# Kernel tuning notes

Measured on AMD Instinct MI355X. Metric: run time of the kernel, lower is better.

The kernel has to match this reference:

```python
import jax, jax.numpy as jnp
import numpy as np


def setup_inputs() -> dict:
    key = jax.random.key(0)
    k1, k2 = jax.random.split(key)
    decoder_state_t = jax.random.normal(k1, (32, 256), dtype=jnp.float32)
    encoder_states = jax.random.normal(k2, (32, 8192, 256), dtype=jnp.float32)
    return {"decoder_state_t": decoder_state_t, "encoder_states": encoder_states}


def reference(decoder_state_t, encoder_states):
    # score[b, s] = sum_h decoder_state_t[b, h] * encoder_states[b, s, h]
    score = jnp.einsum("bh,bsh->bs", decoder_state_t, encoder_states)
    atten_prob = jax.nn.softmax(score, axis=-1)            # (bs, source_length)
    # context[b, h] = sum_s atten_prob[b, s] * encoder_states[b, s, h]
    context = jnp.einsum("bs,bsh->bh", atten_prob, encoder_states)
    return (atten_prob, context)
```

## Files before the change

kernel.cpp:

```cpp
#include <hip/hip_runtime.h>
#include <math.h>

#define B_ 32
#define S_ 8192
#define H_ 256
#define CHUNK_ 512
#define WAVES_PB 4
#define WROWS (CHUNK_ / WAVES_PB)
#define TILE_ 16
#define NCHUNK (S_ / CHUNK_)
#define NPART (B_ * NCHUNK * WAVES_PB)
#define PPB (NCHUNK * WAVES_PB)

__global__ __launch_bounds__(256) void
k1_flash(const float* __restrict__ dec, const float* __restrict__ enc,
         float* __restrict__ scores_out, float* __restrict__ pm,
         float* __restrict__ pl, float* __restrict__ pc) {
    const int lane  = threadIdx.x & 63;
    const int wave  = threadIdx.x >> 6;
    const int batch = blockIdx.x >> 4;
    const int chunk = blockIdx.x & (NCHUNK - 1);
    const int rowBase = chunk * CHUNK_ + wave * WROWS;

    const float4 d = *(const float4*)(dec + batch * H_ + lane * 4);
    const float* ebase = enc + (size_t)batch * S_ * H_;

    float  m = -INFINITY, l = 0.f;
    float4 c = make_float4(0.f, 0.f, 0.f, 0.f);

    for (int t = 0; t < WROWS / TILE_; ++t) {
        const int r0 = rowBase + t * TILE_;
        float4 v[TILE_];
        float  sc[TILE_];
#pragma unroll
        for (int r = 0; r < TILE_; ++r) {
            v[r] = *(const float4*)(ebase + (size_t)(r0 + r) * H_ + lane * 4);
            float sp = v[r].x * d.x + v[r].y * d.y + v[r].z * d.z + v[r].w * d.w;
#pragma unroll
            for (int off = 32; off; off >>= 1) sp += __shfl_xor(sp, off);
            sc[r] = sp;
        }
        float tmax = sc[0];
#pragma unroll
        for (int r = 1; r < TILE_; ++r) tmax = fmaxf(tmax, sc[r]);
        const float mnew = fmaxf(m, tmax);
        const float f = __expf(m - mnew);
        c.x *= f; c.y *= f; c.z *= f; c.w *= f;
        l *= f;
        m = mnew;
#pragma unroll
        for (int r = 0; r < TILE_; ++r) {
            const float p = __expf(sc[r] - m);
            l += p;
            c.x += p * v[r].x;
            c.y += p * v[r].y;
            c.z += p * v[r].z;
            c.w += p * v[r].w;
        }
        if (lane == 0) {
            float* so = scores_out + batch * S_ + r0;
            *(float4*)(so + 0)  = make_float4(sc[0],  sc[1],  sc[2],  sc[3]);
            *(float4*)(so + 4)  = make_float4(sc[4],  sc[5],  sc[6],  sc[7]);
            *(float4*)(so + 8)  = make_float4(sc[8],  sc[9],  sc[10], sc[11]);
            *(float4*)(so + 12) = make_float4(sc[12], sc[13], sc[14], sc[15]);
        }
    }

    const int pid = blockIdx.x * WAVES_PB + wave;
    *(float4*)(pc + (size_t)pid * H_ + lane * 4) = c;
    if (lane == 0) { pm[pid] = m; pl[pid] = l; }
}

__global__ __launch_bounds__(256) void
k23_finish(const float* __restrict__ pm, const float* __restrict__ pl,
           const float* __restrict__ pc, float* __restrict__ probs,
           float* __restrict__ ctx_out) {
    const int lane = threadIdx.x & 63;

    if (blockIdx.x < 256) {
        const int b = blockIdx.x >> 3;
        const float pmv = pm[b * PPB + lane];
        const float plv = pl[b * PPB + lane];
        float M = pmv;
#pragma unroll
        for (int off = 32; off; off >>= 1) M = fmaxf(M, __shfl_xor(M, off));
        float Lp = __expf(pmv - M) * plv;
#pragma unroll
        for (int off = 32; off; off >>= 1) Lp += __shfl_xor(Lp, off);
        const float R = 1.f / Lp;

        float* p = probs + b * S_ + (blockIdx.x & 7) * 1024 + threadIdx.x * 4;
        float4 v = *(const float4*)p;
        v.x = __expf(v.x - M) * R;
        v.y = __expf(v.y - M) * R;
        v.z = __expf(v.z - M) * R;
        v.w = __expf(v.w - M) * R;
        *(float4*)p = v;
    } else {
        const int b = blockIdx.x - 256;
        const int h = threadIdx.x;
        const float pmv = pm[b * PPB + lane];
        const float plv = pl[b * PPB + lane];
        float M = pmv;
#pragma unroll
        for (int off = 32; off; off >>= 1) M = fmaxf(M, __shfl_xor(M, off));
        const float w = __expf(pmv - M);
        float L = w * plv;
#pragma unroll
        for (int off = 32; off; off >>= 1) L += __shfl_xor(L, off);

        float acc = 0.f;
        const float* pcb = pc + (size_t)b * PPB * H_ + h;
#pragma unroll 8
        for (int i = 0; i < PPB; ++i) {
            acc += __shfl(w, i) * pcb[(size_t)i * H_];
        }
        ctx_out[b * H_ + h] = acc / L;
    }
}

extern "C" void kernel_launch(void* const* d_in, const int* in_sizes, int n_in,
                              void* d_out, int out_size, void* d_ws, size_t ws_size,
                              hipStream_t stream) {
    const float* dec = (const float*)d_in[0];
    const float* enc = (const float*)d_in[1];
    float* out    = (float*)d_out;
    float* scores = out;
    float* ctx    = out + B_ * S_;

    float* pm = (float*)d_ws;
    float* pl = pm + NPART;
    float* pc = pl + NPART;

    k1_flash<<<B_ * NCHUNK, 256, 0, stream>>>(dec, enc, scores, pm, pl, pc);
    k23_finish<<<256 + B_, 256, 0, stream>>>(pm, pl, pc, scores, ctx);
}
```

Measured before the change: 52.15 us.

## Fuse flash partial pass and finish into one cooperative kernel with grid sync

Merges the two kernels into a single cooperative launch. A grid-wide barrier separates the partial softmax/context pass from the normalization and context reduction, and each block then normalizes its own chunk of probabilities while chunk-0 blocks reduce the context through shared memory. This removes the second launch and the inter-kernel gap. In exchange it adds the cost of the grid barrier and the cooperative launch, and the 512-block grid must be co-resident for the barrier to work.

```diff
diff --git a/kernel.cpp b/kernel.cpp
--- a/kernel.cpp
+++ b/kernel.cpp
@@ -1,5 +1,8 @@
 #include <hip/hip_runtime.h>
+#include <hip/hip_cooperative_groups.h>
 #include <math.h>
+
+namespace cg = cooperative_groups;
 
 #define B_ 32
 #define S_ 8192
@@ -12,10 +15,11 @@
 #define NPART (B_ * NCHUNK * WAVES_PB)
 #define PPB (NCHUNK * WAVES_PB)
 
-__global__ __launch_bounds__(256) void
-k1_flash(const float* __restrict__ dec, const float* __restrict__ enc,
-         float* __restrict__ scores_out, float* __restrict__ pm,
-         float* __restrict__ pl, float* __restrict__ pc) {
+__global__ __launch_bounds__(256, 2) void
+k_coop(const float* __restrict__ dec, const float* __restrict__ enc,
+       float* __restrict__ probs, float* __restrict__ ctx_out,
+       float* __restrict__ pm, float* __restrict__ pl,
+       float* __restrict__ pc) {
     const int lane  = threadIdx.x & 63;
     const int wave  = threadIdx.x >> 6;
     const int batch = blockIdx.x >> 4;
@@ -58,7 +62,7 @@
             c.w += p * v[r].w;
         }
         if (lane == 0) {
-            float* so = scores_out + batch * S_ + r0;
+            float* so = probs + batch * S_ + r0;
             *(float4*)(so + 0)  = make_float4(sc[0],  sc[1],  sc[2],  sc[3]);
             *(float4*)(so + 4)  = make_float4(sc[4],  sc[5],  sc[6],  sc[7]);
             *(float4*)(so + 8)  = make_float4(sc[8],  sc[9],  sc[10], sc[11]);
@@ -69,53 +73,54 @@
     const int pid = blockIdx.x * WAVES_PB + wave;
     *(float4*)(pc + (size_t)pid * H_ + lane * 4) = c;
     if (lane == 0) { pm[pid] = m; pl[pid] = l; }
-}
 
-__global__ __launch_bounds__(256) void
-k23_finish(const float* __restrict__ pm, const float* __restrict__ pl,
-           const float* __restrict__ pc, float* __restrict__ probs,
-           float* __restrict__ ctx_out) {
-    const int lane = threadIdx.x & 63;
+    cg::this_grid().sync();
 
-    if (blockIdx.x < 256) {
-        const int b = blockIdx.x >> 3;
-        const float pmv = pm[b * PPB + lane];
-        const float plv = pl[b * PPB + lane];
-        float M = pmv;
+    const float pmv = pm[batch * PPB + lane];
+    const float plv = pl[batch * PPB + lane];
+    float M = pmv;
 #pragma unroll
-        for (int off = 32; off; off >>= 1) M = fmaxf(M, __shfl_xor(M, off));
-        float Lp = __expf(pmv - M) * plv;
+    for (int off = 32; off; off >>= 1) M = fmaxf(M, __shfl_xor(M, off));
+    const float w = __expf(pmv - M);
+    float L = w * plv;
 #pragma unroll
-        for (int off = 32; off; off >>= 1) Lp += __shfl_xor(Lp, off);
-        const float R = 1.f / Lp;
+    for (int off = 32; off; off >>= 1) L += __shfl_xor(L, off);
+    const float R = 1.f / L;
 
-        float* p = probs + b * S_ + (blockIdx.x & 7) * 1024 + threadIdx.x * 4;
-        float4 v = *(const float4*)p;
+    if (threadIdx.x < 128) {
+        float4* p = (float4*)(probs + batch * S_ + chunk * CHUNK_) + threadIdx.x;
+        float4 v = *p;
         v.x = __expf(v.x - M) * R;
         v.y = __expf(v.y - M) * R;
         v.z = __expf(v.z - M) * R;
         v.w = __expf(v.w - M) * R;
-        *(float4*)p = v;
-    } else {
-        const int b = blockIdx.x - 256;
-        const int h = threadIdx.x;
-        const float pmv = pm[b * PPB + lane];
-        const float plv = pl[b * PPB + lane];
-        float M = pmv;
+        *p = v;
+    }
+
+    if (chunk == 0) {
+        __shared__ float4 smc[WAVES_PB][64];
+        float4 a4 = make_float4(0.f, 0.f, 0.f, 0.f);
+        const float* pcb = pc + (size_t)batch * PPB * H_;
 #pragma unroll
-        for (int off = 32; off; off >>= 1) M = fmaxf(M, __shfl_xor(M, off));
-        const float w = __expf(pmv - M);
-        float L = w * plv;
+        for (int j = 0; j < PPB / WAVES_PB; ++j) {
+            const int i = wave * (PPB / WAVES_PB) + j;
+            const float wi = __shfl(w, i);
+            const float4 vv = *(const float4*)(pcb + (size_t)i * H_ + lane * 4);
+            a4.x += wi * vv.x; a4.y += wi * vv.y;
+            a4.z += wi * vv.z; a4.w += wi * vv.w;
+        }
+        smc[wave][lane] = a4;
+        __syncthreads();
+        if (wave == 0) {
+            float4 s = smc[0][lane];
 #pragma unroll
-        for (int off = 32; off; off >>= 1) L += __shfl_xor(L, off);
-
-        float acc = 0.f;
-        const float* pcb = pc + (size_t)b * PPB * H_ + h;
-#pragma unroll 8
-        for (int i = 0; i < PPB; ++i) {
-            acc += __shfl(w, i) * pcb[(size_t)i * H_];
+            for (int i = 1; i < WAVES_PB; ++i) {
+                s.x += smc[i][lane].x; s.y += smc[i][lane].y;
+                s.z += smc[i][lane].z; s.w += smc[i][lane].w;
+            }
+            s.x *= R; s.y *= R; s.z *= R; s.w *= R;
+            *(float4*)(ctx_out + batch * H_ + lane * 4) = s;
         }
-        ctx_out[b * H_ + h] = acc / L;
     }
 }
 
@@ -124,14 +129,16 @@
                               hipStream_t stream) {
     const float* dec = (const float*)d_in[0];
     const float* enc = (const float*)d_in[1];
-    float* out    = (float*)d_out;
-    float* scores = out;
-    float* ctx    = out + B_ * S_;
+    float* out   = (float*)d_out;
+    float* probs = out;
+    float* ctx   = out + B_ * S_;
 
     float* pm = (float*)d_ws;
     float* pl = pm + NPART;
     float* pc = pl + NPART;
 
-    k1_flash<<<B_ * NCHUNK, 256, 0, stream>>>(dec, enc, scores, pm, pl, pc);
-    k23_finish<<<256 + B_, 256, 0, stream>>>(pm, pl, pc, scores, ctx);
+    void* args[] = {(void*)&dec, (void*)&enc, (void*)&probs, (void*)&ctx,
+                    (void*)&pm, (void*)&pl, (void*)&pc};
+    hipLaunchCooperativeKernel((void*)k_coop, dim3(B_ * NCHUNK), dim3(256),
+                               args, 0, stream);
 }
```

Result: slower. 114.9 us (+120.4%).

## Halve chunk size and merge wave partials in-block via shared memory

Applied to the files above, without the earlier changes.

The chunk per block drops from 512 to 256 rows, doubling the grid to 1024 blocks so more CUs stay busy while streaming the encoder tensor. The four waves of each block now merge their online-softmax partial (max, sum, context) through shared memory, so each block writes one partial instead of four. The finish kernel then reduces 32 partials per batch instead of 64 and multiplies by a reciprocal. This adds two block barriers and some LDS traffic at the end of the first kernel.

```diff
diff --git a/kernel.cpp b/kernel.cpp
--- a/kernel.cpp
+++ b/kernel.cpp
@@ -4,13 +4,13 @@
 #define B_ 32
 #define S_ 8192
 #define H_ 256
-#define CHUNK_ 512
+#define CHUNK_ 256
 #define WAVES_PB 4
 #define WROWS (CHUNK_ / WAVES_PB)
 #define TILE_ 16
 #define NCHUNK (S_ / CHUNK_)
-#define NPART (B_ * NCHUNK * WAVES_PB)
-#define PPB (NCHUNK * WAVES_PB)
+#define NBLK (B_ * NCHUNK)
+#define PPB NCHUNK
 
 __global__ __launch_bounds__(256) void
 k1_flash(const float* __restrict__ dec, const float* __restrict__ enc,
@@ -18,7 +18,7 @@
          float* __restrict__ pl, float* __restrict__ pc) {
     const int lane  = threadIdx.x & 63;
     const int wave  = threadIdx.x >> 6;
-    const int batch = blockIdx.x >> 4;
+    const int batch = blockIdx.x >> 5;
     const int chunk = blockIdx.x & (NCHUNK - 1);
     const int rowBase = chunk * CHUNK_ + wave * WROWS;
 
@@ -66,9 +66,30 @@
         }
     }
 
-    const int pid = blockIdx.x * WAVES_PB + wave;
-    *(float4*)(pc + (size_t)pid * H_ + lane * 4) = c;
-    if (lane == 0) { pm[pid] = m; pl[pid] = l; }
+    __shared__ float  sm_m[WAVES_PB], sm_l[WAVES_PB];
+    __shared__ float4 smc[WAVES_PB][64];
+    if (lane == 0) { sm_m[wave] = m; sm_l[wave] = l; }
+    __syncthreads();
+    const float Mb = fmaxf(fmaxf(sm_m[0], sm_m[1]), fmaxf(sm_m[2], sm_m[3]));
+    const float wv = __expf(m - Mb);
+    smc[wave][lane] = make_float4(c.x * wv, c.y * wv, c.z * wv, c.w * wv);
+    __syncthreads();
+    if (wave == 0) {
+        float4 s = smc[0][lane];
+#pragma unroll
+        for (int i = 1; i < WAVES_PB; ++i) {
+            s.x += smc[i][lane].x; s.y += smc[i][lane].y;
+            s.z += smc[i][lane].z; s.w += smc[i][lane].w;
+        }
+        *(float4*)(pc + (size_t)blockIdx.x * H_ + lane * 4) = s;
+    }
+    if (threadIdx.x == 0) {
+        float Lb = 0.f;
+#pragma unroll
+        for (int i = 0; i < WAVES_PB; ++i) Lb += __expf(sm_m[i] - Mb) * sm_l[i];
+        pm[blockIdx.x] = Mb;
+        pl[blockIdx.x] = Lb;
+    }
 }
 
 __global__ __launch_bounds__(256) void
@@ -76,19 +97,20 @@
            const float* __restrict__ pc, float* __restrict__ probs,
            float* __restrict__ ctx_out) {
     const int lane = threadIdx.x & 63;
+    const int b = (blockIdx.x < 256) ? (blockIdx.x >> 3) : (blockIdx.x - 256);
+
+    const float pmv = (lane < PPB) ? pm[b * PPB + lane] : -INFINITY;
+    const float plv = (lane < PPB) ? pl[b * PPB + lane] : 0.f;
+    float M = pmv;
+#pragma unroll
+    for (int off = 32; off; off >>= 1) M = fmaxf(M, __shfl_xor(M, off));
+    const float w = __expf(pmv - M);
+    float L = w * plv;
+#pragma unroll
+    for (int off = 32; off; off >>= 1) L += __shfl_xor(L, off);
+    const float R = 1.f / L;
 
     if (blockIdx.x < 256) {
-        const int b = blockIdx.x >> 3;
-        const float pmv = pm[b * PPB + lane];
-        const float plv = pl[b * PPB + lane];
-        float M = pmv;
-#pragma unroll
-        for (int off = 32; off; off >>= 1) M = fmaxf(M, __shfl_xor(M, off));
-        float Lp = __expf(pmv - M) * plv;
-#pragma unroll
-        for (int off = 32; off; off >>= 1) Lp += __shfl_xor(Lp, off);
-        const float R = 1.f / Lp;
-
         float* p = probs + b * S_ + (blockIdx.x & 7) * 1024 + threadIdx.x * 4;
         float4 v = *(const float4*)p;
         v.x = __expf(v.x - M) * R;
@@ -97,25 +119,13 @@
         v.w = __expf(v.w - M) * R;
         *(float4*)p = v;
     } else {
-        const int b = blockIdx.x - 256;
         const int h = threadIdx.x;
-        const float pmv = pm[b * PPB + lane];
-        const float plv = pl[b * PPB + lane];
-        float M = pmv;
-#pragma unroll
-        for (int off = 32; off; off >>= 1) M = fmaxf(M, __shfl_xor(M, off));
-        const float w = __expf(pmv - M);
-        float L = w * plv;
-#pragma unroll
-        for (int off = 32; off; off >>= 1) L += __shfl_xor(L, off);
-
         float acc = 0.f;
         const float* pcb = pc + (size_t)b * PPB * H_ + h;
 #pragma unroll 8
-        for (int i = 0; i < PPB; ++i) {
+        for (int i = 0; i < PPB; ++i)
             acc += __shfl(w, i) * pcb[(size_t)i * H_];
-        }
-        ctx_out[b * H_ + h] = acc / L;
+        ctx_out[b * H_ + h] = acc * R;
     }
 }
 
@@ -124,14 +134,14 @@
                               hipStream_t stream) {
     const float* dec = (const float*)d_in[0];
     const float* enc = (const float*)d_in[1];
-    float* out    = (float*)d_out;
-    float* scores = out;
-    float* ctx    = out + B_ * S_;
+    float* out   = (float*)d_out;
+    float* probs = out;
+    float* ctx   = out + B_ * S_;
 
     float* pm = (float*)d_ws;
-    float* pl = pm + NPART;
-    float* pc = pl + NPART;
+    float* pl = pm + NBLK;
+    float* pc = pl + NBLK;
 
-    k1_flash<<<B_ * NCHUNK, 256, 0, stream>>>(dec, enc, scores, pm, pl, pc);
-    k23_finish<<<256 + B_, 256, 0, stream>>>(pm, pl, pc, scores, ctx);
+    k1_flash<<<NBLK, 256, 0, stream>>>(dec, enc, probs, pm, pl, pc);
+    k23_finish<<<256 + B_, 256, 0, stream>>>(pm, pl, pc, probs, ctx);
 }
```

Result: faster. 50.67 us (-2.8%).
